# Kernel tuning notes

Hardware: AMD Instinct MI355X
Metric: run time of the kernel (lower is better)

The kernel has to match this reference:

```python
import jax, jax.numpy as jnp
import numpy as np

V = 32000   # vocab_size
C = 64      # n_embd
H = 4       # n_head
S = 16      # head_size (H*S == C)
T = 128     # block_size == seq len
B = 2       # batch
HID = 256   # hidden_size = 4*C
L = 1       # n_layer
NPE = 4     # pe1..pe4


def _ln(x, g, b, eps=1e-5):
    m = jnp.mean(x, -1, keepdims=True)
    v = jnp.mean((x - m) ** 2, -1, keepdims=True)
    return (x - m) * jax.lax.rsqrt(v + eps) * g + b


def setup_inputs() -> dict:
    key = jax.random.key(0)
    ks = jax.random.split(key, 16)
    r = lambda i, shape: jax.random.normal(ks[i], shape, jnp.float32) * 0.02
    inp = {}
    inp['idx'] = jax.random.randint(ks[0], (B, T), 0, V)
    inp['tok_emb'] = r(1, (V, C))
    # 4 independent PositionalEmbedding modules (stacked on leading axis)
    inp['pe_tables'] = r(2, (NPE, T, C))
    inp['pe_ff_W1'] = r(3, (NPE, C, C)); inp['pe_ff_b1'] = jnp.zeros((NPE, C))
    inp['pe_ff_W2'] = r(4, (NPE, C, C)); inp['pe_ff_b2'] = jnp.zeros((NPE, C))
    inp['pe_ln_g'] = jnp.ones((NPE, C)); inp['pe_ln_b'] = jnp.zeros((NPE, C))
    # Block params (stacked on layer axis L)
    inp['ln1_g'] = jnp.ones((L, C)); inp['ln1_b'] = jnp.zeros((L, C))
    inp['att_W1'] = r(5, (L, H, 4 * C, 4 * C)); inp['att_b1'] = jnp.zeros((L, H, 4 * C))
    inp['att_W2'] = r(6, (L, H, 4 * C)); inp['att_b2'] = jnp.zeros((L, H))
    inp['val_W'] = r(7, (L, H, C, S))
    inp['proj_W'] = r(8, (L, C, C)); inp['proj_b'] = jnp.zeros((L, C))
    inp['ln2_g'] = jnp.ones((L, C)); inp['ln2_b'] = jnp.zeros((L, C))
    inp['ff_W1'] = r(9, (L, C, HID)); inp['ff_b1'] = jnp.zeros((L, HID))
    inp['ff_W2'] = r(10, (L, HID, C)); inp['ff_b2'] = jnp.zeros((L, C))
    inp['ln3_g'] = jnp.ones((L, C)); inp['ln3_b'] = jnp.zeros((L, C))
    inp['lm_W'] = r(11, (C, V)); inp['lm_b'] = jnp.zeros((V,))
    return inp


def reference(idx, tok_emb, pe_tables, pe_ff_W1, pe_ff_b1, pe_ff_W2, pe_ff_b2,
              pe_ln_g, pe_ln_b, ln1_g, ln1_b, att_W1, att_b1, att_W2, att_b2,
              val_W, proj_W, proj_b, ln2_g, ln2_b, ff_W1, ff_b1, ff_W2, ff_b2,
              ln3_g, ln3_b, lm_W, lm_b):
    b, t = idx.shape
    x = tok_emb[idx]                               # [b,t,C]
    tril = jnp.tril(jnp.ones((t, t), bool))

    # PositionalEmbedding: table -> FFN(sigmoid) -> LayerNorm (independent of x values)
    def pos_embed(p):
        pe = jnp.broadcast_to(pe_tables[p, :t][None], (b, t, C))
        h = jax.nn.sigmoid(pe @ pe_ff_W1[p] + pe_ff_b1[p])
        pe = h @ pe_ff_W2[p] + pe_ff_b2[p]
        return _ln(pe, pe_ln_g[p], pe_ln_b[p])

    def block(x, pos_emb, l):
        xn = _ln(x, ln1_g[l], ln1_b[l])
        x1 = jnp.concatenate([pos_emb, xn], -1)     # [b,t,2C]
        # att2 first Linear is linear in cat([k,q]) -> split weight into k/q halves
        W1k = att_W1[l][:, :2 * C, :]               # [H,2C,4C] (acts on x1[j])
        W1q = att_W1[l][:, 2 * C:, :]               # [H,2C,4C] (acts on x1[i])
        Kp = jnp.einsum('btc,hcd->hbtd', x1, W1k)   # [H,b,t,4C]
        Qp = jnp.einsum('btc,hcd->hbtd', x1, W1q)
        hid = jax.nn.sigmoid(Qp[:, :, :, None, :] + Kp[:, :, None, :, :]
                             + att_b1[l][:, None, None, None, :])  # [H,b,t,t,4C]
        scores = jnp.einsum('hbijd,hd->hbij', hid, att_W2[l]) + att_b2[l][:, None, None, None]
        wei = scores * (C ** -0.5)
        wei = jnp.where(tril[None, None], wei, float('-inf'))
        wei = jax.nn.softmax(wei, -1)               # [H,b,t,t]
        v = jnp.einsum('btc,hcs->hbts', xn, val_W[l])
        o = jnp.einsum('hbij,hbjs->hbis', wei, v)   # [H,b,t,S]
        o = jnp.transpose(o, (1, 2, 0, 3)).reshape(b, t, H * S)
        x = x + (o @ proj_W[l] + proj_b[l])
        xn2 = _ln(x, ln2_g[l], ln2_b[l])
        ff = jax.nn.sigmoid(xn2 @ ff_W1[l] + ff_b1[l]) @ ff_W2[l] + ff_b2[l]
        x = x + ff
        return _ln(x, ln3_g[l], ln3_b[l])

    # Same BlockSequence applied 4 times, each with a fresh positional embedding
    for p in range(NPE):
        pos = pos_embed(p)
        for l in range(L):
            x = block(x, pos, l)

    return x @ lm_W + lm_b                          # [b,t,V]
```

## Files before the change

kernel.cpp:

```cpp
#include <hip/hip_runtime.h>

#define TT    128
#define CC    64
#define HH    4
#define SS    16
#define D4    256
#define HID_  256
#define VV    32000
#define NPE_  4
#define RR    256
#define LOG2E 1.44269504f

__device__ __forceinline__ float wred_sum(float v) {
#pragma unroll
    for (int off = 32; off; off >>= 1) v += __shfl_xor(v, off, 64);
    return v;
}
__device__ __forceinline__ float wred_max(float v) {
#pragma unroll
    for (int off = 32; off; off >>= 1) v = fmaxf(v, __shfl_xor(v, off, 64));
    return v;
}
__device__ __forceinline__ float sigm(float x) {
    return __builtin_amdgcn_rcpf(1.f + exp2f(-x * LOG2E));
}
__device__ __forceinline__ float sigm2(float t) {
    return __builtin_amdgcn_rcpf(1.f + exp2f(-t));
}

#define DPP_ADD(v, ctrl)                                                       \
    v += __int_as_float(__builtin_amdgcn_update_dpp(                           \
        0, __float_as_int(v), ctrl, 0xF, 0xF, true))
__device__ __forceinline__ float row16_sum(float v) {
    DPP_ADD(v, 0x128);
    DPP_ADD(v, 0x124);
    DPP_ADD(v, 0x122);
    DPP_ADD(v, 0x121);
    return v;
}

__global__ void k_embed_pos(const int* __restrict__ idx, const float* __restrict__ tok,
                            const float* __restrict__ pe_tab, const float* __restrict__ W1,
                            const float* __restrict__ b1, const float* __restrict__ W2,
                            const float* __restrict__ b2, const float* __restrict__ g,
                            const float* __restrict__ bb,
                            float* __restrict__ x, float* __restrict__ pos) {
    int blk = blockIdx.x, c = threadIdx.x;
    if (blk >= 512) {
        int r = blk - 512;
        x[r * CC + c] = tok[idx[r] * CC + c];
        return;
    }
    int p = blk >> 7, t = blk & 127;
    __shared__ float s_pe[CC], s_h[CC];
    s_pe[c] = pe_tab[(p * TT + t) * CC + c];
    __syncthreads();
    const float* w1 = W1 + p * CC * CC;
    float a = b1[p * CC + c];
    for (int k = 0; k < CC; k++) a += s_pe[k] * w1[k * CC + c];
    s_h[c] = sigm(a);
    __syncthreads();
    const float* w2 = W2 + p * CC * CC;
    float o = b2[p * CC + c];
    for (int k = 0; k < CC; k++) o += s_h[k] * w2[k * CC + c];
    float m = wred_sum(o) * (1.f / CC);
    float d = o - m;
    float var = wred_sum(d * d) * (1.f / CC);
    pos[(p * TT + t) * CC + c] =
        d * rsqrtf(var + 1e-5f) * g[p * CC + c] + bb[p * CC + c];
}

__global__ void __launch_bounds__(256) k_stageA(
    const float* __restrict__ x, const float* __restrict__ pos_p,
    const float* __restrict__ ln1g, const float* __restrict__ ln1b,
    const float* __restrict__ attW1, const float* __restrict__ ab1,
    const float* __restrict__ valW,
    float* __restrict__ Kp, float* __restrict__ Qp, float* __restrict__ v) {
    int blk = blockIdx.x, tid = threadIdx.x;
    int lane = tid & 63, wv = tid >> 6;
    int rg = blk & 31, kq = (blk >> 5) & 1, h = blk >> 6;
    int r0 = rg * 8;
    __shared__ __align__(16) float x1[8][128];
#pragma unroll
    for (int pass = 0; pass < 2; ++pass) {
        int rr = wv + pass * 4;
        float xv = x[(r0 + rr) * CC + lane];
        float m = wred_sum(xv) * (1.f / CC);
        float d = xv - m;
        float var = wred_sum(d * d) * (1.f / CC);
        x1[rr][64 + lane] = d * rsqrtf(var + 1e-5f) * ln1g[lane] + ln1b[lane];
    }
    for (int e = tid; e < 512; e += 256) {
        int rr = e >> 6, cc = e & 63;
        int t = (r0 + rr) & (TT - 1);
        x1[rr][cc] = pos_p[t * CC + cc];
    }
    __syncthreads();
    const float* w = attW1 + (h * D4 + kq * 128) * D4 + tid;
    float a0 = 0, a1 = 0, a2 = 0, a3 = 0, a4 = 0, a5 = 0, a6 = 0, a7 = 0;
    for (int c = 0; c < 128; c += 4) {
        float4 xr0 = *(const float4*)&x1[0][c];
        float4 xr1 = *(const float4*)&x1[1][c];
        float4 xr2 = *(const float4*)&x1[2][c];
        float4 xr3 = *(const float4*)&x1[3][c];
        float4 xr4 = *(const float4*)&x1[4][c];
        float4 xr5 = *(const float4*)&x1[5][c];
        float4 xr6 = *(const float4*)&x1[6][c];
        float4 xr7 = *(const float4*)&x1[7][c];
        float w0 = w[(size_t)(c + 0) * D4];
        float w1 = w[(size_t)(c + 1) * D4];
        float w2 = w[(size_t)(c + 2) * D4];
        float w3 = w[(size_t)(c + 3) * D4];
        a0 += xr0.x * w0 + xr0.y * w1 + xr0.z * w2 + xr0.w * w3;
        a1 += xr1.x * w0 + xr1.y * w1 + xr1.z * w2 + xr1.w * w3;
        a2 += xr2.x * w0 + xr2.y * w1 + xr2.z * w2 + xr2.w * w3;
        a3 += xr3.x * w0 + xr3.y * w1 + xr3.z * w2 + xr3.w * w3;
        a4 += xr4.x * w0 + xr4.y * w1 + xr4.z * w2 + xr4.w * w3;
        a5 += xr5.x * w0 + xr5.y * w1 + xr5.z * w2 + xr5.w * w3;
        a6 += xr6.x * w0 + xr6.y * w1 + xr6.z * w2 + xr6.w * w3;
        a7 += xr7.x * w0 + xr7.y * w1 + xr7.z * w2 + xr7.w * w3;
    }
    float badd = kq ? 0.f : ab1[h * D4 + tid];
    float* outKQ = kq ? Qp : Kp;
    outKQ[(h * RR + r0 + 0) * D4 + tid] = (a0 + badd) * LOG2E;
    outKQ[(h * RR + r0 + 1) * D4 + tid] = (a1 + badd) * LOG2E;
    outKQ[(h * RR + r0 + 2) * D4 + tid] = (a2 + badd) * LOG2E;
    outKQ[(h * RR + r0 + 3) * D4 + tid] = (a3 + badd) * LOG2E;
    outKQ[(h * RR + r0 + 4) * D4 + tid] = (a4 + badd) * LOG2E;
    outKQ[(h * RR + r0 + 5) * D4 + tid] = (a5 + badd) * LOG2E;
    outKQ[(h * RR + r0 + 6) * D4 + tid] = (a6 + badd) * LOG2E;
    outKQ[(h * RR + r0 + 7) * D4 + tid] = (a7 + badd) * LOG2E;
    if (kq == 0 && tid < 128) {
        int rr = tid >> 4, s = tid & 15;
        const float* wvw = valW + h * CC * SS;
        float a = 0.f;
        for (int k = 0; k < CC; k++) a += x1[rr][64 + k] * wvw[k * SS + s];
        v[(h * RR + r0 + rr) * SS + s] = a;
    }
}

__global__ void __launch_bounds__(256) k_att3(
    const float* __restrict__ Kp, const float* __restrict__ Qp,
    const float* __restrict__ v,
    const float* __restrict__ aw2, const float* __restrict__ ab2,
    float* __restrict__ o) {
    int bid = blockIdx.x;
    int row = bid & 255, h = bid >> 8;
    int bat = row >> 7, i = row & 127;
    int tid = threadIdx.x, lane = tid & 63, wv = tid >> 6;
    __shared__ float sc[TT];
    __shared__ float part[16][17];
    {
        int sub = lane >> 4;
        int dlo = (lane & 15) * 16;
        const float* qrow = Qp + (size_t)(h * RR + row) * D4 + dlo;
        float4 q0 = *(const float4*)(qrow + 0);
        float4 q1 = *(const float4*)(qrow + 4);
        float4 q2 = *(const float4*)(qrow + 8);
        float4 q3 = *(const float4*)(qrow + 12);
        const float* wrow = aw2 + h * D4 + dlo;
        float4 w0 = *(const float4*)(wrow + 0);
        float4 w1 = *(const float4*)(wrow + 4);
        float4 w2 = *(const float4*)(wrow + 8);
        float4 w3 = *(const float4*)(wrow + 12);
        const float sc8 = 0.125f;
        w0.x *= sc8; w0.y *= sc8; w0.z *= sc8; w0.w *= sc8;
        w1.x *= sc8; w1.y *= sc8; w1.z *= sc8; w1.w *= sc8;
        w2.x *= sc8; w2.y *= sc8; w2.z *= sc8; w2.w *= sc8;
        w3.x *= sc8; w3.y *= sc8; w3.z *= sc8; w3.w *= sc8;
        float b2s = ab2[h] * 0.125f;
        const float* Kb = Kp + (size_t)(h * RR + bat * TT) * D4 + dlo;
        for (int j = wv * 4 + sub; j <= i; j += 16) {
            const float* kj = Kb + (size_t)j * D4;
            float4 k0 = *(const float4*)(kj + 0);
            float4 k1 = *(const float4*)(kj + 4);
            float4 k2 = *(const float4*)(kj + 8);
            float4 k3 = *(const float4*)(kj + 12);
            float p = 0.f;
            p += sigm2(q0.x + k0.x) * w0.x + sigm2(q0.y + k0.y) * w0.y +
                 sigm2(q0.z + k0.z) * w0.z + sigm2(q0.w + k0.w) * w0.w;
            p += sigm2(q1.x + k1.x) * w1.x + sigm2(q1.y + k1.y) * w1.y +
                 sigm2(q1.z + k1.z) * w1.z + sigm2(q1.w + k1.w) * w1.w;
            p += sigm2(q2.x + k2.x) * w2.x + sigm2(q2.y + k2.y) * w2.y +
                 sigm2(q2.z + k2.z) * w2.z + sigm2(q2.w + k2.w) * w2.w;
            p += sigm2(q3.x + k3.x) * w3.x + sigm2(q3.y + k3.y) * w3.y +
                 sigm2(q3.z + k3.z) * w3.z + sigm2(q3.w + k3.w) * w3.w;
            p = row16_sum(p);
            if ((lane & 15) == 0) sc[j] = p + b2s;
        }
    }
    __syncthreads();
    int jg = wv;
    if (jg == 0) {
        float s0 = (lane <= i) ? sc[lane] : -1e30f;
        float s1 = (lane + 64 <= i) ? sc[lane + 64] : -1e30f;
        float m = wred_max(fmaxf(s0, s1));
        float e0 = (lane <= i) ? __expf(s0 - m) : 0.f;
        float e1 = (lane + 64 <= i) ? __expf(s1 - m) : 0.f;
        float inv = __builtin_amdgcn_rcpf(wred_sum(e0 + e1));
        sc[lane] = e0 * inv;
        sc[lane + 64] = e1 * inv;
    }
    __syncthreads();
    {
        int jo = lane >> 4, s = lane & 15;
        int jstart = jg * 4 + jo;
        const float* vb = v + (h * RR + bat * TT) * SS;
        float acc = 0.f;
        for (int j = jstart; j <= i; j += 16) acc += sc[j] * vb[j * SS + s];
        part[jstart][s] = acc;
    }
    __syncthreads();
    if (tid < 16) {
        float a = 0.f;
#pragma unroll
        for (int k = 0; k < 16; ++k) a += part[k][tid];
        o[row * CC + h * SS + tid] = a;
    }
}

__global__ void __launch_bounds__(256) k_post(
    float* __restrict__ x, const float* __restrict__ o,
    const float* __restrict__ projW, const float* __restrict__ projb,
    const float* __restrict__ g2, const float* __restrict__ b2,
    const float* __restrict__ fW1, const float* __restrict__ fb1,
    const float* __restrict__ fW2, const float* __restrict__ fb2,
    const float* __restrict__ g3, const float* __restrict__ b3) {
    int row = blockIdx.x, tid = threadIdx.x;
    __shared__ float o_s[CC], s_x[CC], s_h[HID_], red[4][CC];
    if (tid < CC) o_s[tid] = o[row * CC + tid];
    __syncthreads();
    {
        int c = tid & 63, q = tid >> 6;
        float a0 = 0.f, a1 = 0.f;
        int k0 = q * 16;
#pragma unroll
        for (int k = 0; k < 16; k += 2) {
            a0 += o_s[k0 + k] * projW[(k0 + k) * CC + c];
            a1 += o_s[k0 + k + 1] * projW[(k0 + k + 1) * CC + c];
        }
        red[q][c] = a0 + a1;
    }
    __syncthreads();
    float xv = 0.f;
    if (tid < CC) {
        xv = x[row * CC + tid] + projb[tid] +
             red[0][tid] + red[1][tid] + red[2][tid] + red[3][tid];
        float m = wred_sum(xv) * (1.f / CC);
        float d = xv - m;
        float var = wred_sum(d * d) * (1.f / CC);
        s_x[tid] = d * rsqrtf(var + 1e-5f) * g2[tid] + b2[tid];
    }
    __syncthreads();
    {
        float a0 = fb1[tid], a1 = 0.f;
#pragma unroll
        for (int k = 0; k < CC; k += 2) {
            a0 += s_x[k] * fW1[k * HID_ + tid];
            a1 += s_x[k + 1] * fW1[(k + 1) * HID_ + tid];
        }
        s_h[tid] = sigm(a0 + a1);
    }
    __syncthreads();
    {
        int c = tid & 63, q = tid >> 6;
        float a0 = 0.f, a1 = 0.f;
#pragma unroll
        for (int k = q * 64; k < q * 64 + 64; k += 2) {
            a0 += s_h[k] * fW2[k * CC + c];
            a1 += s_h[k + 1] * fW2[(k + 1) * CC + c];
        }
        red[q][c] = a0 + a1;
    }
    __syncthreads();
    if (tid < CC) {
        float f = fb2[tid] + red[0][tid] + red[1][tid] + red[2][tid] + red[3][tid];
        float x2 = xv + f;
        float m = wred_sum(x2) * (1.f / CC);
        float d = x2 - m;
        float var = wred_sum(d * d) * (1.f / CC);
        x[row * CC + tid] = d * rsqrtf(var + 1e-5f) * g3[tid] + b3[tid];
    }
}

__device__ __forceinline__ void lm_fma(float4& acc, float xs, float4 wv) {
    acc.x += xs * wv.x; acc.y += xs * wv.y;
    acc.z += xs * wv.z; acc.w += xs * wv.w;
}
__global__ void __launch_bounds__(256, 2) k_lmhead(const float* __restrict__ x,
                                                   const float* __restrict__ lmW,
                                                   const float* __restrict__ lmb,
                                                   float* __restrict__ out) {
    int tid = threadIdx.x;
    int r0 = blockIdx.y * 8;
    __shared__ __align__(16) float xT[CC][8];
    for (int e = tid; e < 8 * CC; e += 256) {
        int r = e >> 6, c = e & 63;
        xT[c][r] = x[(r0 + r) * CC + c];
    }
    __syncthreads();
    if (tid >= 250) return;
    int v8 = blockIdx.x * 2000 + tid * 8;
    float4 b0 = *(const float4*)(lmb + v8);
    float4 b1 = *(const float4*)(lmb + v8 + 4);
    float4 c0r0 = b0, c0r1 = b0, c0r2 = b0, c0r3 = b0;
    float4 c0r4 = b0, c0r5 = b0, c0r6 = b0, c0r7 = b0;
    float4 c1r0 = b1, c1r1 = b1, c1r2 = b1, c1r3 = b1;
    float4 c1r4 = b1, c1r5 = b1, c1r6 = b1, c1r7 = b1;
#pragma unroll 4
    for (int c = 0; c < CC; ++c) {
        float4 w0 = *(const float4*)(lmW + (size_t)c * VV + v8);
        float4 w1 = *(const float4*)(lmW + (size_t)c * VV + v8 + 4);
        float4 xa = *(const float4*)&xT[c][0];
        float4 xb = *(const float4*)&xT[c][4];
        lm_fma(c0r0, xa.x, w0); lm_fma(c0r1, xa.y, w0);
        lm_fma(c0r2, xa.z, w0); lm_fma(c0r3, xa.w, w0);
        lm_fma(c0r4, xb.x, w0); lm_fma(c0r5, xb.y, w0);
        lm_fma(c0r6, xb.z, w0); lm_fma(c0r7, xb.w, w0);
        lm_fma(c1r0, xa.x, w1); lm_fma(c1r1, xa.y, w1);
        lm_fma(c1r2, xa.z, w1); lm_fma(c1r3, xa.w, w1);
        lm_fma(c1r4, xb.x, w1); lm_fma(c1r5, xb.y, w1);
        lm_fma(c1r6, xb.z, w1); lm_fma(c1r7, xb.w, w1);
    }
    float* ob = out + (size_t)r0 * VV + v8;
    *(float4*)(ob + 0 * VV) = c0r0; *(float4*)(ob + 0 * VV + 4) = c1r0;
    *(float4*)(ob + 1 * VV) = c0r1; *(float4*)(ob + 1 * VV + 4) = c1r1;
    *(float4*)(ob + 2 * VV) = c0r2; *(float4*)(ob + 2 * VV + 4) = c1r2;
    *(float4*)(ob + 3 * VV) = c0r3; *(float4*)(ob + 3 * VV + 4) = c1r3;
    *(float4*)(ob + 4 * VV) = c0r4; *(float4*)(ob + 4 * VV + 4) = c1r4;
    *(float4*)(ob + 5 * VV) = c0r5; *(float4*)(ob + 5 * VV + 4) = c1r5;
    *(float4*)(ob + 6 * VV) = c0r6; *(float4*)(ob + 6 * VV + 4) = c1r6;
    *(float4*)(ob + 7 * VV) = c0r7; *(float4*)(ob + 7 * VV + 4) = c1r7;
}

extern "C" void kernel_launch(void* const* d_in, const int* in_sizes, int n_in,
                              void* d_out, int out_size, void* d_ws, size_t ws_size,
                              hipStream_t stream) {
    const int*   idx   = (const int*)d_in[0];
    const float* tok   = (const float*)d_in[1];
    const float* petab = (const float*)d_in[2];
    const float* peW1  = (const float*)d_in[3];
    const float* peb1  = (const float*)d_in[4];
    const float* peW2  = (const float*)d_in[5];
    const float* peb2  = (const float*)d_in[6];
    const float* peg   = (const float*)d_in[7];
    const float* pebb  = (const float*)d_in[8];
    const float* ln1g  = (const float*)d_in[9];
    const float* ln1b  = (const float*)d_in[10];
    const float* attW1 = (const float*)d_in[11];
    const float* attb1 = (const float*)d_in[12];
    const float* attW2 = (const float*)d_in[13];
    const float* attb2 = (const float*)d_in[14];
    const float* valW  = (const float*)d_in[15];
    const float* projW = (const float*)d_in[16];
    const float* projb = (const float*)d_in[17];
    const float* ln2g  = (const float*)d_in[18];
    const float* ln2b  = (const float*)d_in[19];
    const float* ffW1  = (const float*)d_in[20];
    const float* ffb1  = (const float*)d_in[21];
    const float* ffW2  = (const float*)d_in[22];
    const float* ffb2  = (const float*)d_in[23];
    const float* ln3g  = (const float*)d_in[24];
    const float* ln3b  = (const float*)d_in[25];
    const float* lmW   = (const float*)d_in[26];
    const float* lmb   = (const float*)d_in[27];

    float* ws  = (float*)d_ws;
    float* x   = ws;
    float* pos = ws + 16384;
    float* v   = ws + 49152;
    float* o   = ws + 65536;
    float* Kp  = ws + 81920;
    float* Qp  = ws + 344064;

    k_embed_pos<<<768, CC, 0, stream>>>(idx, tok, petab, peW1, peb1, peW2, peb2,
                                        peg, pebb, x, pos);
    for (int p = 0; p < NPE_; p++) {
        k_stageA<<<256, 256, 0, stream>>>(x, pos + p * TT * CC, ln1g, ln1b,
                                          attW1, attb1, valW, Kp, Qp, v);
        k_att3<<<HH * RR, 256, 0, stream>>>(Kp, Qp, v, attW2, attb2, o);
        k_post<<<RR, 256, 0, stream>>>(x, o, projW, projb, ln2g, ln2b,
                                       ffW1, ffb1, ffW2, ffb2, ln3g, ln3b);
    }
    k_lmhead<<<dim3(16, 32), 256, 0, stream>>>(x, lmW, lmb, (float*)d_out);
}
```

Measured before the change: 159.5 us.

## Pair causal rows i and 127-i per block to balance attention work

The attention kernel now handles two query rows per block, i and 127-i, using 512 threads, so every block covers about the same number of causal keys. Before, each block handled a single row and the work per block grew with the row index. Weight loads and scaling are hoisted and shared across both rows, and the grid is halved to 512 blocks. In exchange, blocks are larger, which may reduce occupancy flexibility, and each row gets fewer waves per key.

```diff
diff --git a/kernel.cpp b/kernel.cpp
--- a/kernel.cpp
+++ b/kernel.cpp
@@ -139,38 +139,41 @@
     }
 }
 
-__global__ void __launch_bounds__(256) k_att3(
+__global__ void __launch_bounds__(512) k_att4(
     const float* __restrict__ Kp, const float* __restrict__ Qp,
     const float* __restrict__ v,
     const float* __restrict__ aw2, const float* __restrict__ ab2,
     float* __restrict__ o) {
     int bid = blockIdx.x;
-    int row = bid & 255, h = bid >> 8;
-    int bat = row >> 7, i = row & 127;
+    int pairIdx = bid & 63, bat = (bid >> 6) & 1, h = bid >> 7;
+    int iA = pairIdx, iB = 127 - pairIdx;
     int tid = threadIdx.x, lane = tid & 63, wv = tid >> 6;
-    __shared__ float sc[TT];
-    __shared__ float part[16][17];
-    {
-        int sub = lane >> 4;
-        int dlo = (lane & 15) * 16;
+    __shared__ float sc[2][TT];
+    __shared__ float part[2][16][17];
+    int sub = lane >> 4;
+    int dlo = (lane & 15) * 16;
+    const float* wrow = aw2 + h * D4 + dlo;
+    float4 w0 = *(const float4*)(wrow + 0);
+    float4 w1 = *(const float4*)(wrow + 4);
+    float4 w2 = *(const float4*)(wrow + 8);
+    float4 w3 = *(const float4*)(wrow + 12);
+    const float sc8 = 0.125f;
+    w0.x *= sc8; w0.y *= sc8; w0.z *= sc8; w0.w *= sc8;
+    w1.x *= sc8; w1.y *= sc8; w1.z *= sc8; w1.w *= sc8;
+    w2.x *= sc8; w2.y *= sc8; w2.z *= sc8; w2.w *= sc8;
+    w3.x *= sc8; w3.y *= sc8; w3.z *= sc8; w3.w *= sc8;
+    float b2s = ab2[h] * 0.125f;
+    const float* Kb = Kp + (size_t)(h * RR + bat * TT) * D4 + dlo;
+#pragma unroll
+    for (int rsel = 0; rsel < 2; ++rsel) {
+        int i = rsel ? iB : iA;
+        int row = bat * TT + i;
         const float* qrow = Qp + (size_t)(h * RR + row) * D4 + dlo;
         float4 q0 = *(const float4*)(qrow + 0);
         float4 q1 = *(const float4*)(qrow + 4);
         float4 q2 = *(const float4*)(qrow + 8);
         float4 q3 = *(const float4*)(qrow + 12);
-        const float* wrow = aw2 + h * D4 + dlo;
-        float4 w0 = *(const float4*)(wrow + 0);
-        float4 w1 = *(const float4*)(wrow + 4);
-        float4 w2 = *(const float4*)(wrow + 8);
-        float4 w3 = *(const float4*)(wrow + 12);
-        const float sc8 = 0.125f;
-        w0.x *= sc8; w0.y *= sc8; w0.z *= sc8; w0.w *= sc8;
-        w1.x *= sc8; w1.y *= sc8; w1.z *= sc8; w1.w *= sc8;
-        w2.x *= sc8; w2.y *= sc8; w2.z *= sc8; w2.w *= sc8;
-        w3.x *= sc8; w3.y *= sc8; w3.z *= sc8; w3.w *= sc8;
-        float b2s = ab2[h] * 0.125f;
-        const float* Kb = Kp + (size_t)(h * RR + bat * TT) * D4 + dlo;
-        for (int j = wv * 4 + sub; j <= i; j += 16) {
+        for (int j = wv * 4 + sub; j <= i; j += 32) {
             const float* kj = Kb + (size_t)j * D4;
             float4 k0 = *(const float4*)(kj + 0);
             float4 k1 = *(const float4*)(kj + 4);
@@ -186,36 +189,42 @@
             p += sigm2(q3.x + k3.x) * w3.x + sigm2(q3.y + k3.y) * w3.y +
                  sigm2(q3.z + k3.z) * w3.z + sigm2(q3.w + k3.w) * w3.w;
             p = row16_sum(p);
-            if ((lane & 15) == 0) sc[j] = p + b2s;
+            if ((lane & 15) == 0) sc[rsel][j] = p + b2s;
         }
     }
     __syncthreads();
-    int jg = wv;
-    if (jg == 0) {
-        float s0 = (lane <= i) ? sc[lane] : -1e30f;
-        float s1 = (lane + 64 <= i) ? sc[lane + 64] : -1e30f;
+    if ((wv & 3) == 0) {
+        int rsel = wv >> 2;
+        int i = rsel ? iB : iA;
+        float s0 = (lane <= i) ? sc[rsel][lane] : -1e30f;
+        float s1 = (lane + 64 <= i) ? sc[rsel][lane + 64] : -1e30f;
         float m = wred_max(fmaxf(s0, s1));
         float e0 = (lane <= i) ? __expf(s0 - m) : 0.f;
         float e1 = (lane + 64 <= i) ? __expf(s1 - m) : 0.f;
         float inv = __builtin_amdgcn_rcpf(wred_sum(e0 + e1));
-        sc[lane] = e0 * inv;
-        sc[lane + 64] = e1 * inv;
+        sc[rsel][lane] = e0 * inv;
+        sc[rsel][lane + 64] = e1 * inv;
     }
     __syncthreads();
     {
+        int rsel = wv >> 2, wq = wv & 3;
+        int i = rsel ? iB : iA;
         int jo = lane >> 4, s = lane & 15;
-        int jstart = jg * 4 + jo;
-        const float* vb = v + (h * RR + bat * TT) * SS;
+        int jstart = wq * 4 + jo;
+        const float* vb = v + (size_t)(h * RR + bat * TT) * SS;
         float acc = 0.f;
-        for (int j = jstart; j <= i; j += 16) acc += sc[j] * vb[j * SS + s];
-        part[jstart][s] = acc;
-    }
-    __syncthreads();
-    if (tid < 16) {
+        for (int j = jstart; j <= i; j += 16) acc += sc[rsel][j] * vb[j * SS + s];
+        part[rsel][jstart][s] = acc;
+    }
+    __syncthreads();
+    if (tid < 32) {
+        int rsel = tid >> 4, s = tid & 15;
+        int i = rsel ? iB : iA;
+        int row = bat * TT + i;
         float a = 0.f;
 #pragma unroll
-        for (int k = 0; k < 16; ++k) a += part[k][tid];
-        o[row * CC + h * SS + tid] = a;
+        for (int k = 0; k < 16; ++k) a += part[rsel][k][s];
+        o[row * CC + h * SS + s] = a;
     }
 }
 
@@ -378,7 +387,7 @@
     for (int p = 0; p < NPE_; p++) {
         k_stageA<<<256, 256, 0, stream>>>(x, pos + p * TT * CC, ln1g, ln1b,
                                           attW1, attb1, valW, Kp, Qp, v);
-        k_att3<<<HH * RR, 256, 0, stream>>>(Kp, Qp, v, attW2, attb2, o);
+        k_att4<<<512, 512, 0, stream>>>(Kp, Qp, v, attW2, attb2, o);
         k_post<<<RR, 256, 0, stream>>>(x, o, projW, projb, ln2g, ln2b,
                                        ffW1, ffb1, ffW2, ffb2, ln3g, ln3b);
     }
```

New measurement: 142.9 us. -10.4%, faster.
